# Kernel tuning notes

Measured on AMD Instinct MI355X. Metric: run time of the kernel, lower is better.

## Reference

```python
import jax, jax.numpy as jnp
import numpy as np

N = 20000   # nodes
E = 640000  # edges (avg degree 32)
D = 128     # feature dim
BN_EPS = 1e-5


def setup_inputs() -> dict:
    key = jax.random.key(0)
    ks = jax.random.split(key, 24)
    s = 1.0 / np.sqrt(D)
    inp = {
        'h': jax.random.normal(ks[0], (N, D), jnp.float32),
        'e': jax.random.normal(ks[1], (E, D), jnp.float32),
        'src': jax.random.randint(ks[2], (E,), 0, N, jnp.int32),
        'dst': jax.random.randint(ks[3], (E,), 0, N, jnp.int32),
        'Wa': jax.random.normal(ks[4], (D, D), jnp.float32) * s,
        'ba': jnp.zeros((D,), jnp.float32),
        'Wb': jax.random.normal(ks[5], (D, D), jnp.float32) * s,
        'bb': jnp.zeros((D,), jnp.float32),
        'Wc': jax.random.normal(ks[6], (D, D), jnp.float32) * s,
        'bc': jnp.zeros((D,), jnp.float32),
        'Wd': jax.random.normal(ks[7], (D, D), jnp.float32) * s,
        'bd': jnp.zeros((D,), jnp.float32),
        'We': jax.random.normal(ks[8], (D, D), jnp.float32) * s,
        'be': jnp.zeros((D,), jnp.float32),
        'gamma_h': jnp.ones((D,), jnp.float32),
        'beta_h': jnp.zeros((D,), jnp.float32),
        'mean_h': jax.random.normal(ks[9], (D,), jnp.float32) * 0.1,
        'var_h': jax.random.uniform(ks[10], (D,), jnp.float32) + 0.5,
        'gamma_e': jnp.ones((D,), jnp.float32),
        'beta_e': jnp.zeros((D,), jnp.float32),
        'mean_e': jax.random.normal(ks[11], (D,), jnp.float32) * 0.1,
        'var_e': jax.random.uniform(ks[12], (D,), jnp.float32) + 0.5,
    }
    return inp


def reference(h, e, src, dst, Wa, ba, Wb, bb, Wc, bc, Wd, bd, We, be,
              gamma_h, beta_h, mean_h, var_h, gamma_e, beta_e, mean_e, var_e):
    # Node/edge linear projections (same as Linear: x @ W.T + b)
    Ah = h @ Wa.T + ba
    Bh = h @ Wb.T + bb
    Dh = h @ Wd.T + bd
    Eh = h @ We.T + be
    Ce = e @ Wc.T + bc

    # Edge gate: e_ij = Ce + Dh[src] + Eh[dst]
    e_new = Ce + Dh[src] + Eh[dst]          # [E, D]
    sigma = jax.nn.sigmoid(e_new)           # [E, D]

    # Normalized gated aggregation over incoming edges at each destination node
    num = jax.ops.segment_sum(sigma * Bh[src], dst, num_segments=N)  # [N, D]
    den = jax.ops.segment_sum(sigma, dst, num_segments=N)            # [N, D]
    h_new = Ah + num / (den + 1e-6)

    # BatchNorm (inference form, as written in the torch forward) + ReLU
    h_out = jax.nn.relu(gamma_h * (h_new - mean_h) / jnp.sqrt(var_h + BN_EPS) + beta_h)
    e_out = jax.nn.relu(gamma_e * (e_new - mean_e) / jnp.sqrt(var_e + BN_EPS) + beta_e)
    return h_out, e_out
```

## Files before the change

### kernel.cpp

```cpp
#include <hip/hip_runtime.h>

#define NN 20000
#define NE 640000
#define DIM 128
#define ND (NN * DIM)

typedef float f32x4 __attribute__((ext_vector_type(4)));
typedef __bf16 bf16x4 __attribute__((ext_vector_type(4)));
typedef __bf16 bf16x8 __attribute__((ext_vector_type(8)));

__device__ __forceinline__ int swz(int r, int c) {
  return r * DIM + (c ^ ((r & 7) << 3));
}
__device__ __forceinline__ int swzr(int r, int c) {
  return r * DIM + (c ^ ((r & 3) << 3) ^ (((r >> 2) & 3) << 4));
}

__global__ void prep(const float* __restrict__ Wa, const float* __restrict__ Wb,
                     const float* __restrict__ Wd, const float* __restrict__ We,
                     const float* __restrict__ Wc, __bf16* __restrict__ wbf,
                     __bf16* __restrict__ wcp,
                     const float* __restrict__ gh, const float* __restrict__ bh,
                     const float* __restrict__ mh, const float* __restrict__ vh,
                     const float* __restrict__ ge, const float* __restrict__ be_,
                     const float* __restrict__ me, const float* __restrict__ ve,
                     float* __restrict__ bn) {
  int b = blockIdx.x;
  int tid = threadIdx.x;
  if (b < 256) {
    int g = b * 256 + tid;
    int m = g >> 14;
    int off = g & 16383;
    const float* s = (m == 0) ? Wa : (m == 1) ? Wb : (m == 2) ? Wd : We;
    wbf[g] = (__bf16)s[off];
    if (g < DIM) {
      float sc = gh[g] * rsqrtf(vh[g] + 1e-5f);
      bn[g] = sc;
      bn[DIM + g] = bh[g] - mh[g] * sc;
    } else if (g < 2 * DIM) {
      int c = g - DIM;
      float sc = ge[c] * rsqrtf(ve[c] + 1e-5f);
      bn[2 * DIM + c] = sc;
      bn[3 * DIM + c] = be_[c] - me[c] * sc;
    }
  } else {
    int t2 = (b - 256) * 256 + tid;
    int lane = t2 & 63, nt = (t2 >> 6) & 7, ks = t2 >> 9;
    int lq = lane >> 4, lm = lane & 15;
    const float* srcp = Wc + (nt * 16 + lm) * DIM + ks * 32 + lq * 8;
    bf16x8 v;
#pragma unroll
    for (int j = 0; j < 8; ++j) v[j] = (__bf16)srcp[j];
    *(bf16x8*)(wcp + t2 * 8) = v;
  }
}

__global__ void hist(const int* __restrict__ dst, int* __restrict__ cur) {
  int e = blockIdx.x * 256 + threadIdx.x;
  if (e < NE) atomicAdd(cur + dst[e], 1);
}

__global__ __launch_bounds__(1024) void scan20k(int* __restrict__ cur) {
  __shared__ int wsum[16];
  int tid = threadIdx.x;
  int wid = tid >> 6, lane = tid & 63;
  int carry = 0;
  for (int base = 0; base < NN; base += 1024) {
    int i = base + tid;
    int v = (i < NN) ? cur[i] : 0;
    int x = v;
#pragma unroll
    for (int d = 1; d < 64; d <<= 1) {
      int y = __shfl_up(x, d, 64);
      if (lane >= d) x += y;
    }
    if (lane == 63) wsum[wid] = x;
    __syncthreads();
    if (wid == 0 && lane < 16) {
      int s = wsum[lane];
#pragma unroll
      for (int d = 1; d < 16; d <<= 1) {
        int y = __shfl_up(s, d, 64);
        if (lane >= d) s += y;
      }
      wsum[lane] = s;
    }
    __syncthreads();
    int woff = (wid > 0) ? wsum[wid - 1] : 0;
    if (i < NN) cur[i] = carry + woff + x - v;
    carry += wsum[15];
    __syncthreads();
  }
}

__global__ void scatter(const int* __restrict__ dst, int* __restrict__ cur,
                        int* __restrict__ perm) {
  int e = blockIdx.x * 256 + threadIdx.x;
  if (e < NE) {
    int p = atomicAdd(cur + dst[e], 1);
    perm[p] = e;
  }
}

__global__ __launch_bounds__(256) void node_gemm(
    const float* __restrict__ h, const __bf16* __restrict__ wbf,
    const float* __restrict__ ba, const float* __restrict__ bb,
    const float* __restrict__ bd, const float* __restrict__ be,
    float* __restrict__ Ah, __bf16* __restrict__ Bhb,
    __bf16* __restrict__ Dhb, __bf16* __restrict__ Ehb) {
  __shared__ __bf16 As[64 * DIM];
  __shared__ __bf16 Ws[DIM * DIM];
  const int tid = threadIdx.x;
  const int row0 = blockIdx.x * 64;

#pragma unroll
  for (int it = 0; it < 8; ++it) {
    int flat = it * 1024 + tid * 4;
    int r = flat >> 7, c = flat & 127;
    int grow = row0 + r;
    f32x4 v;
    if (grow < NN) v = *(const f32x4*)(h + grow * DIM + c);
    else v = (f32x4){0.f, 0.f, 0.f, 0.f};
    bf16x4 b;
    b[0] = (__bf16)v[0]; b[1] = (__bf16)v[1];
    b[2] = (__bf16)v[2]; b[3] = (__bf16)v[3];
    *(bf16x4*)(As + swz(r, c)) = b;
  }

  const int wv = tid >> 6, lane = tid & 63;
  const int lq = lane >> 4, lm = lane & 15;

#pragma unroll 1
  for (int m = 0; m < 4; ++m) {
    __syncthreads();
#pragma unroll
    for (int it = 0; it < 8; ++it) {
      int chunk = it * 256 + tid;
      int r = chunk >> 4, c0 = (chunk & 15) << 3;
      bf16x8 v = *(const bf16x8*)(wbf + m * DIM * DIM + (chunk << 3));
      *(bf16x8*)(Ws + swz(r, c0)) = v;
    }
    __syncthreads();

    f32x4 acc[8];
#pragma unroll
    for (int i = 0; i < 8; ++i) acc[i] = (f32x4){0.f, 0.f, 0.f, 0.f};
#pragma unroll
    for (int ks = 0; ks < 4; ++ks) {
      int k0 = ks * 32 + lq * 8;
      int ar = wv * 16 + lm;
      bf16x8 a = *(const bf16x8*)(As + swz(ar, k0));
#pragma unroll
      for (int nt = 0; nt < 8; ++nt) {
        int bcol = nt * 16 + lm;
        bf16x8 b = *(const bf16x8*)(Ws + swz(bcol, k0));
        acc[nt] = __builtin_amdgcn_mfma_f32_16x16x32_bf16(a, b, acc[nt], 0, 0, 0);
      }
    }
    const float* bias = (m == 0) ? ba : (m == 1) ? bb : (m == 2) ? bd : be;
#pragma unroll
    for (int nt = 0; nt < 8; ++nt) {
      int col = nt * 16 + lm;
      float bv = bias[col];
#pragma unroll
      for (int r = 0; r < 4; ++r) {
        int grow = row0 + wv * 16 + lq * 4 + r;
        if (grow < NN) {
          float val = acc[nt][r] + bv;
          if (m == 0) Ah[grow * DIM + col] = val;
          else if (m == 1) Bhb[grow * DIM + col] = (__bf16)val;
          else if (m == 2) Dhb[grow * DIM + col] = (__bf16)val;
          else Ehb[grow * DIM + col] = (__bf16)val;
        }
      }
    }
  }
}

union SmemU {
  __bf16 As[64 * DIM];
  struct { __bf16 sg[64 * DIM]; __bf16 sb[64 * DIM]; } r;
};

__global__ __launch_bounds__(256, 4) void edge_gemm(
    const float* __restrict__ e, const __bf16* __restrict__ wcp,
    const int* __restrict__ src, const int* __restrict__ dst,
    const int* __restrict__ perm, const float* __restrict__ bc,
    const __bf16* __restrict__ Bhb, const __bf16* __restrict__ Dhb,
    const __bf16* __restrict__ Ehb,
    float* __restrict__ num, float* __restrict__ den,
    float* __restrict__ e_out, const float* __restrict__ bn) {
  __shared__ SmemU u;
  __shared__ int s_perm[64], s_src[64], s_dst[64];
  const int tid = threadIdx.x;
  const int e0 = blockIdx.x * 64;

  if (tid < 64) {
    int p = perm[e0 + tid];
    s_perm[tid] = p;
    s_src[tid] = src[p];
    s_dst[tid] = dst[p];
  }
  __syncthreads();

#pragma unroll
  for (int it = 0; it < 8; ++it) {
    int flat = it * 1024 + tid * 4;
    int r = flat >> 7, c = flat & 127;
    f32x4 v = __builtin_nontemporal_load(
        (const f32x4*)(e + (size_t)s_perm[r] * DIM + c));
    bf16x4 b;
    b[0] = (__bf16)v[0]; b[1] = (__bf16)v[1];
    b[2] = (__bf16)v[2]; b[3] = (__bf16)v[3];
    *(bf16x4*)(u.As + swz(r, c)) = b;
  }
  __syncthreads();

  const int wv = tid >> 6, lane = tid & 63;
  const int lq = lane >> 4, lm = lane & 15;

  f32x4 acc[8];
#pragma unroll
  for (int i = 0; i < 8; ++i) acc[i] = (f32x4){0.f, 0.f, 0.f, 0.f};
  const bf16x8* wp = (const bf16x8*)wcp;
#pragma unroll
  for (int ks = 0; ks < 4; ++ks) {
    int k0 = ks * 32 + lq * 8;
    int ar = wv * 16 + lm;
    bf16x8 a = *(const bf16x8*)(u.As + swz(ar, k0));
#pragma unroll
    for (int nt = 0; nt < 8; ++nt) {
      bf16x8 b = wp[(ks * 8 + nt) * 64 + lane];
      acc[nt] = __builtin_amdgcn_mfma_f32_16x16x32_bf16(a, b, acc[nt], 0, 0, 0);
    }
  }
  __syncthreads();

  const float* scale_e = bn + 2 * DIM;
  const float* shift_e = bn + 3 * DIM;
#pragma unroll
  for (int nt = 0; nt < 8; ++nt) {
    int col = nt * 16 + lm;
    float bcv = bc[col];
    float sc = scale_e[col], sh = shift_e[col];
#pragma unroll
    for (int r = 0; r < 4; ++r) {
      int lrow = wv * 16 + lq * 4 + r;
      int s = s_src[lrow];
      float x = acc[nt][r] + bcv + (float)Dhb[s * DIM + col]
              + (float)Ehb[s_dst[lrow] * DIM + col];
      float sig = 1.0f / (1.0f + __expf(-x));
      __builtin_nontemporal_store(fmaxf(sc * x + sh, 0.0f),
                                  e_out + (size_t)s_perm[lrow] * DIM + col);
      int a = swzr(lrow, col);
      u.r.sg[a] = (__bf16)sig;
      u.r.sb[a] = (__bf16)(sig * (float)Bhb[s * DIM + col]);
    }
  }
  __syncthreads();

  {
    int col = tid >> 1;
    int r0 = (tid & 1) << 5;
    float an = 0.f, ad = 0.f;
    int prev = s_dst[r0];
#pragma unroll 4
    for (int k = 0; k < 32; ++k) {
      int row = r0 + k;
      int d = s_dst[row];
      if (d != prev) {
        atomicAdd(num + (size_t)prev * DIM + col, an);
        atomicAdd(den + (size_t)prev * DIM + col, ad);
        an = 0.f; ad = 0.f; prev = d;
      }
      int a = swzr(row, col);
      an += (float)u.r.sb[a];
      ad += (float)u.r.sg[a];
    }
    atomicAdd(num + (size_t)prev * DIM + col, an);
    atomicAdd(den + (size_t)prev * DIM + col, ad);
  }
}

__global__ void final_h(const float* __restrict__ Ah, const float* __restrict__ num,
                        const float* __restrict__ den, const float* __restrict__ bn,
                        float* __restrict__ h_out) {
  int g = blockIdx.x * blockDim.x + threadIdx.x;
  int idx = g * 4;
  int col = idx & (DIM - 1);
  f32x4 a = *(const f32x4*)(Ah + idx);
  f32x4 n = *(const f32x4*)(num + idx);
  f32x4 d = *(const f32x4*)(den + idx);
  f32x4 o;
#pragma unroll
  for (int j = 0; j < 4; ++j) {
    float hn = a[j] + n[j] / (d[j] + 1e-6f);
    o[j] = fmaxf(bn[col + j] * hn + bn[DIM + col + j], 0.0f);
  }
  *(f32x4*)(h_out + idx) = o;
}

extern "C" void kernel_launch(void* const* d_in, const int* in_sizes, int n_in,
                              void* d_out, int out_size, void* d_ws, size_t ws_size,
                              hipStream_t stream) {
  (void)in_sizes; (void)n_in; (void)out_size; (void)ws_size;
  const float* h   = (const float*)d_in[0];
  const float* e   = (const float*)d_in[1];
  const int*   src = (const int*)d_in[2];
  const int*   dst = (const int*)d_in[3];
  const float* Wa  = (const float*)d_in[4];
  const float* ba  = (const float*)d_in[5];
  const float* Wb  = (const float*)d_in[6];
  const float* bb  = (const float*)d_in[7];
  const float* Wc  = (const float*)d_in[8];
  const float* bc  = (const float*)d_in[9];
  const float* Wd  = (const float*)d_in[10];
  const float* bd  = (const float*)d_in[11];
  const float* We  = (const float*)d_in[12];
  const float* be  = (const float*)d_in[13];
  const float* gamma_h = (const float*)d_in[14];
  const float* beta_h  = (const float*)d_in[15];
  const float* mean_h  = (const float*)d_in[16];
  const float* var_h   = (const float*)d_in[17];
  const float* gamma_e = (const float*)d_in[18];
  const float* beta_e  = (const float*)d_in[19];
  const float* mean_e  = (const float*)d_in[20];
  const float* var_e   = (const float*)d_in[21];

  float* ws  = (float*)d_ws;
  float* Ah  = ws;
  float* num = Ah + ND;
  float* den = num + ND;
  __bf16* Bhb = (__bf16*)(den + ND);
  __bf16* Dhb = Bhb + ND;
  __bf16* Ehb = Dhb + ND;
  __bf16* wbf = Ehb + ND;
  __bf16* wcp = wbf + 4 * DIM * DIM;
  float* bn  = (float*)(wcp + DIM * DIM);
  int*   cur = (int*)(bn + 4 * DIM);
  int*   perm = cur + NN;

  float* h_out = (float*)d_out;
  float* e_out = h_out + ND;

  hipMemsetAsync(num, 0, (size_t)2 * ND * sizeof(float), stream);
  hipMemsetAsync(cur, 0, (size_t)NN * sizeof(int), stream);
  prep<<<264, 256, 0, stream>>>(Wa, Wb, Wd, We, Wc, wbf, wcp,
                                gamma_h, beta_h, mean_h, var_h,
                                gamma_e, beta_e, mean_e, var_e, bn);
  hist<<<NE / 256, 256, 0, stream>>>(dst, cur);
  scan20k<<<1, 1024, 0, stream>>>(cur);
  scatter<<<NE / 256, 256, 0, stream>>>(dst, cur, perm);
  node_gemm<<<(NN + 63) / 64, 256, 0, stream>>>(h, wbf, ba, bb, bd, be,
                                                Ah, Bhb, Dhb, Ehb);
  edge_gemm<<<NE / 64, 256, 0, stream>>>(e, wcp, src, dst, perm, bc,
                                         Bhb, Dhb, Ehb, num, den, e_out, bn);
  final_h<<<ND / 4 / 256, 256, 0, stream>>>(Ah, num, den, bn, h_out);
}
```

Measured before the change: 376.0 us.

## Split node GEMM per matrix, fold bc into Dh, use plain stores for interior segments

Node GEMM now launches one block per (row tile, weight matrix), which gives four times more blocks and drops the serial loop over matrices. The edge bias bc is folded into the Dh projection, so the edge kernel no longer adds it. The edge epilogue stores only packed sigmoid values to shared memory and recomputes sigma*Bh in the reduction, which halves shared-memory use. Interior destination segments inside a thread's row chunk use plain stores instead of atomics. Other changes are a vectorized scan, bf16 packing via perm, and rcp in place of division. Together these risk slightly lower precision from rcp, and the plain stores are correct only because all of a node's edges fall inside one chunk in sorted order.

```diff
diff --git a/kernel.cpp b/kernel.cpp
--- a/kernel.cpp
+++ b/kernel.cpp
@@ -8,13 +8,17 @@
 typedef float f32x4 __attribute__((ext_vector_type(4)));
 typedef __bf16 bf16x4 __attribute__((ext_vector_type(4)));
 typedef __bf16 bf16x8 __attribute__((ext_vector_type(8)));
+typedef unsigned int u32;
+typedef u32 u32x2 __attribute__((ext_vector_type(2)));
 
 __device__ __forceinline__ int swz(int r, int c) {
   return r * DIM + (c ^ ((r & 7) << 3));
 }
-__device__ __forceinline__ int swzr(int r, int c) {
-  return r * DIM + (c ^ ((r & 3) << 3) ^ (((r >> 2) & 3) << 4));
-}
+__device__ __forceinline__ u32 pk_bf16(float a, float b) {
+  return __builtin_amdgcn_perm(__float_as_uint(b), __float_as_uint(a), 0x07060302u);
+}
+__device__ __forceinline__ float bf16_lo(u32 w) { return __uint_as_float(w << 16); }
+__device__ __forceinline__ float bf16_hi(u32 w) { return __uint_as_float(w & 0xffff0000u); }
 
 __global__ void prep(const float* __restrict__ Wa, const float* __restrict__ Wb,
                      const float* __restrict__ Wd, const float* __restrict__ We,
@@ -62,13 +66,14 @@
 
 __global__ __launch_bounds__(1024) void scan20k(int* __restrict__ cur) {
   __shared__ int wsum[16];
-  int tid = threadIdx.x;
-  int wid = tid >> 6, lane = tid & 63;
+  int tid = threadIdx.x, wid = tid >> 6, lane = tid & 63;
   int carry = 0;
-  for (int base = 0; base < NN; base += 1024) {
-    int i = base + tid;
-    int v = (i < NN) ? cur[i] : 0;
-    int x = v;
+  for (int base = 0; base < NN; base += 4096) {
+    int idx = base + tid * 4;
+    int4 v = {0, 0, 0, 0};
+    if (idx < NN) v = *(const int4*)(cur + idx);
+    int sum = v.x + v.y + v.z + v.w;
+    int x = sum;
 #pragma unroll
     for (int d = 1; d < 64; d <<= 1) {
       int y = __shfl_up(x, d, 64);
@@ -76,18 +81,22 @@
     }
     if (lane == 63) wsum[wid] = x;
     __syncthreads();
-    if (wid == 0 && lane < 16) {
-      int s = wsum[lane];
+    if (tid < 16) {
+      int s = wsum[tid];
 #pragma unroll
       for (int d = 1; d < 16; d <<= 1) {
         int y = __shfl_up(s, d, 64);
-        if (lane >= d) s += y;
+        if (tid >= d) s += y;
       }
-      wsum[lane] = s;
+      wsum[tid] = s;
     }
     __syncthreads();
-    int woff = (wid > 0) ? wsum[wid - 1] : 0;
-    if (i < NN) cur[i] = carry + woff + x - v;
+    int excl = carry + ((wid > 0) ? wsum[wid - 1] : 0) + x - sum;
+    if (idx < NN) {
+      int4 o;
+      o.x = excl; o.y = excl + v.x; o.z = o.y + v.y; o.w = o.z + v.z;
+      *(int4*)(cur + idx) = o;
+    }
     carry += wsum[15];
     __syncthreads();
   }
@@ -106,72 +115,70 @@
     const float* __restrict__ h, const __bf16* __restrict__ wbf,
     const float* __restrict__ ba, const float* __restrict__ bb,
     const float* __restrict__ bd, const float* __restrict__ be,
+    const float* __restrict__ bc,
     float* __restrict__ Ah, __bf16* __restrict__ Bhb,
     __bf16* __restrict__ Dhb, __bf16* __restrict__ Ehb) {
   __shared__ __bf16 As[64 * DIM];
   __shared__ __bf16 Ws[DIM * DIM];
   const int tid = threadIdx.x;
-  const int row0 = blockIdx.x * 64;
+  const int m = blockIdx.x & 3;
+  const int row0 = (blockIdx.x >> 2) * 64;
 
 #pragma unroll
   for (int it = 0; it < 8; ++it) {
     int flat = it * 1024 + tid * 4;
     int r = flat >> 7, c = flat & 127;
     int grow = row0 + r;
-    f32x4 v;
+    f32x4 v = (f32x4){0.f, 0.f, 0.f, 0.f};
     if (grow < NN) v = *(const f32x4*)(h + grow * DIM + c);
-    else v = (f32x4){0.f, 0.f, 0.f, 0.f};
-    bf16x4 b;
-    b[0] = (__bf16)v[0]; b[1] = (__bf16)v[1];
-    b[2] = (__bf16)v[2]; b[3] = (__bf16)v[3];
-    *(bf16x4*)(As + swz(r, c)) = b;
-  }
+    u32x2 pk;
+    pk[0] = pk_bf16(v[0], v[1]);
+    pk[1] = pk_bf16(v[2], v[3]);
+    *(u32x2*)(As + swz(r, c)) = pk;
+  }
+#pragma unroll
+  for (int it = 0; it < 8; ++it) {
+    int chunk = it * 256 + tid;
+    int r = chunk >> 4, c0 = (chunk & 15) << 3;
+    bf16x8 v = *(const bf16x8*)(wbf + m * DIM * DIM + (chunk << 3));
+    *(bf16x8*)(Ws + swz(r, c0)) = v;
+  }
+  __syncthreads();
 
   const int wv = tid >> 6, lane = tid & 63;
   const int lq = lane >> 4, lm = lane & 15;
 
-#pragma unroll 1
-  for (int m = 0; m < 4; ++m) {
-    __syncthreads();
-#pragma unroll
-    for (int it = 0; it < 8; ++it) {
-      int chunk = it * 256 + tid;
-      int r = chunk >> 4, c0 = (chunk & 15) << 3;
-      bf16x8 v = *(const bf16x8*)(wbf + m * DIM * DIM + (chunk << 3));
-      *(bf16x8*)(Ws + swz(r, c0)) = v;
-    }
-    __syncthreads();
-
-    f32x4 acc[8];
-#pragma unroll
-    for (int i = 0; i < 8; ++i) acc[i] = (f32x4){0.f, 0.f, 0.f, 0.f};
-#pragma unroll
-    for (int ks = 0; ks < 4; ++ks) {
-      int k0 = ks * 32 + lq * 8;
-      int ar = wv * 16 + lm;
-      bf16x8 a = *(const bf16x8*)(As + swz(ar, k0));
-#pragma unroll
-      for (int nt = 0; nt < 8; ++nt) {
-        int bcol = nt * 16 + lm;
-        bf16x8 b = *(const bf16x8*)(Ws + swz(bcol, k0));
-        acc[nt] = __builtin_amdgcn_mfma_f32_16x16x32_bf16(a, b, acc[nt], 0, 0, 0);
-      }
-    }
-    const float* bias = (m == 0) ? ba : (m == 1) ? bb : (m == 2) ? bd : be;
+  f32x4 acc[8];
+#pragma unroll
+  for (int i = 0; i < 8; ++i) acc[i] = (f32x4){0.f, 0.f, 0.f, 0.f};
+#pragma unroll
+  for (int ks = 0; ks < 4; ++ks) {
+    int k0 = ks * 32 + lq * 8;
+    int ar = wv * 16 + lm;
+    bf16x8 a = *(const bf16x8*)(As + swz(ar, k0));
 #pragma unroll
     for (int nt = 0; nt < 8; ++nt) {
-      int col = nt * 16 + lm;
-      float bv = bias[col];
-#pragma unroll
-      for (int r = 0; r < 4; ++r) {
-        int grow = row0 + wv * 16 + lq * 4 + r;
-        if (grow < NN) {
-          float val = acc[nt][r] + bv;
-          if (m == 0) Ah[grow * DIM + col] = val;
-          else if (m == 1) Bhb[grow * DIM + col] = (__bf16)val;
-          else if (m == 2) Dhb[grow * DIM + col] = (__bf16)val;
-          else Ehb[grow * DIM + col] = (__bf16)val;
-        }
+      int bcol = nt * 16 + lm;
+      bf16x8 b = *(const bf16x8*)(Ws + swz(bcol, k0));
+      acc[nt] = __builtin_amdgcn_mfma_f32_16x16x32_bf16(a, b, acc[nt], 0, 0, 0);
+    }
+  }
+
+  const float* bias = (m == 0) ? ba : (m == 1) ? bb : (m == 2) ? bd : be;
+#pragma unroll
+  for (int nt = 0; nt < 8; ++nt) {
+    int col = nt * 16 + lm;
+    float bv = bias[col];
+    if (m == 2) bv += bc[col];
+#pragma unroll
+    for (int r = 0; r < 4; ++r) {
+      int grow = row0 + wv * 16 + lq * 4 + r;
+      if (grow < NN) {
+        float val = acc[nt][r] + bv;
+        if (m == 0) Ah[grow * DIM + col] = val;
+        else if (m == 1) Bhb[grow * DIM + col] = (__bf16)val;
+        else if (m == 2) Dhb[grow * DIM + col] = (__bf16)val;
+        else Ehb[grow * DIM + col] = (__bf16)val;
       }
     }
   }
@@ -179,13 +186,13 @@
 
 union SmemU {
   __bf16 As[64 * DIM];
-  struct { __bf16 sg[64 * DIM]; __bf16 sb[64 * DIM]; } r;
+  u32 sgp[32 * DIM];
 };
 
 __global__ __launch_bounds__(256, 4) void edge_gemm(
     const float* __restrict__ e, const __bf16* __restrict__ wcp,
     const int* __restrict__ src, const int* __restrict__ dst,
-    const int* __restrict__ perm, const float* __restrict__ bc,
+    const int* __restrict__ perm,
     const __bf16* __restrict__ Bhb, const __bf16* __restrict__ Dhb,
     const __bf16* __restrict__ Ehb,
     float* __restrict__ num, float* __restrict__ den,
@@ -209,10 +216,10 @@
     int r = flat >> 7, c = flat & 127;
     f32x4 v = __builtin_nontemporal_load(
         (const f32x4*)(e + (size_t)s_perm[r] * DIM + c));
-    bf16x4 b;
-    b[0] = (__bf16)v[0]; b[1] = (__bf16)v[1];
-    b[2] = (__bf16)v[2]; b[3] = (__bf16)v[3];
-    *(bf16x4*)(u.As + swz(r, c)) = b;
+    u32x2 pk;
+    pk[0] = pk_bf16(v[0], v[1]);
+    pk[1] = pk_bf16(v[2], v[3]);
+    *(u32x2*)(u.As + swz(r, c)) = pk;
   }
   __syncthreads();
 
@@ -241,20 +248,23 @@
 #pragma unroll
   for (int nt = 0; nt < 8; ++nt) {
     int col = nt * 16 + lm;
-    float bcv = bc[col];
     float sc = scale_e[col], sh = shift_e[col];
 #pragma unroll
-    for (int r = 0; r < 4; ++r) {
-      int lrow = wv * 16 + lq * 4 + r;
-      int s = s_src[lrow];
-      float x = acc[nt][r] + bcv + (float)Dhb[s * DIM + col]
-              + (float)Ehb[s_dst[lrow] * DIM + col];
-      float sig = 1.0f / (1.0f + __expf(-x));
-      __builtin_nontemporal_store(fmaxf(sc * x + sh, 0.0f),
-                                  e_out + (size_t)s_perm[lrow] * DIM + col);
-      int a = swzr(lrow, col);
-      u.r.sg[a] = (__bf16)sig;
-      u.r.sb[a] = (__bf16)(sig * (float)Bhb[s * DIM + col]);
+    for (int j = 0; j < 2; ++j) {
+      int lrow = wv * 16 + lq * 4 + 2 * j;
+      float g2[2];
+#pragma unroll
+      for (int t = 0; t < 2; ++t) {
+        int row = lrow + t;
+        int s = s_src[row];
+        float x = acc[nt][2 * j + t] + (float)Dhb[s * DIM + col]
+                + (float)Ehb[s_dst[row] * DIM + col];
+        g2[t] = __builtin_amdgcn_rcpf(1.0f + __expf(-x));
+        __builtin_nontemporal_store(fmaxf(sc * x + sh, 0.0f),
+                                    e_out + (size_t)s_perm[row] * DIM + col);
+      }
+      int wr = wv * 8 + lq * 2 + j;
+      u.sgp[wr * DIM + ((col + wr * 8) & 127)] = pk_bf16(g2[0], g2[1]);
     }
   }
   __syncthreads();
@@ -262,23 +272,36 @@
   {
     int col = tid >> 1;
     int r0 = (tid & 1) << 5;
+    int wrb = (tid & 1) << 4;
     float an = 0.f, ad = 0.f;
     int prev = s_dst[r0];
+    int seg_start = r0;
 #pragma unroll 4
-    for (int k = 0; k < 32; ++k) {
-      int row = r0 + k;
-      int d = s_dst[row];
-      if (d != prev) {
-        atomicAdd(num + (size_t)prev * DIM + col, an);
-        atomicAdd(den + (size_t)prev * DIM + col, ad);
-        an = 0.f; ad = 0.f; prev = d;
+    for (int i = 0; i < 16; ++i) {
+      int wr = wrb + i;
+      u32 w = u.sgp[wr * DIM + ((col + wr * 8) & 127)];
+      float sv0 = bf16_lo(w), sv1 = bf16_hi(w);
+#pragma unroll
+      for (int t = 0; t < 2; ++t) {
+        int row = wr * 2 + t;
+        float sv = t ? sv1 : sv0;
+        int d = s_dst[row];
+        if (d != prev) {
+          if (seg_start > r0) {
+            num[prev * DIM + col] = an;
+            den[prev * DIM + col] = ad;
+          } else {
+            atomicAdd(num + prev * DIM + col, an);
+            atomicAdd(den + prev * DIM + col, ad);
+          }
+          an = 0.f; ad = 0.f; prev = d; seg_start = row;
+        }
+        an += sv * (float)Bhb[s_src[row] * DIM + col];
+        ad += sv;
       }
-      int a = swzr(row, col);
-      an += (float)u.r.sb[a];
-      ad += (float)u.r.sg[a];
-    }
-    atomicAdd(num + (size_t)prev * DIM + col, an);
-    atomicAdd(den + (size_t)prev * DIM + col, ad);
+    }
+    atomicAdd(num + prev * DIM + col, an);
+    atomicAdd(den + prev * DIM + col, ad);
   }
 }
 
@@ -294,7 +317,7 @@
   f32x4 o;
 #pragma unroll
   for (int j = 0; j < 4; ++j) {
-    float hn = a[j] + n[j] / (d[j] + 1e-6f);
+    float hn = a[j] + n[j] * __builtin_amdgcn_rcpf(d[j] + 1e-6f);
     o[j] = fmaxf(bn[col + j] * hn + bn[DIM + col + j], 0.0f);
   }
   *(f32x4*)(h_out + idx) = o;
@@ -351,9 +374,9 @@
   hist<<<NE / 256, 256, 0, stream>>>(dst, cur);
   scan20k<<<1, 1024, 0, stream>>>(cur);
   scatter<<<NE / 256, 256, 0, stream>>>(dst, cur, perm);
-  node_gemm<<<(NN + 63) / 64, 256, 0, stream>>>(h, wbf, ba, bb, bd, be,
-                                                Ah, Bhb, Dhb, Ehb);
-  edge_gemm<<<NE / 64, 256, 0, stream>>>(e, wcp, src, dst, perm, bc,
+  node_gemm<<<((NN + 63) / 64) * 4, 256, 0, stream>>>(h, wbf, ba, bb, bd, be, bc,
+                                                      Ah, Bhb, Dhb, Ehb);
+  edge_gemm<<<NE / 64, 256, 0, stream>>>(e, wcp, src, dst, perm,
                                          Bhb, Dhb, Ehb, num, den, e_out, bn);
   final_h<<<ND / 4 / 256, 256, 0, stream>>>(Ah, num, den, bn, h_out);
 }
```

Measured after the change: 421.3 us. 12.1% more time.
